# Performance work log

Hardware: AMD Instinct MI355X
Metric: run time of the kernel (lower is better)

## Reference

```python
import jax, jax.numpy as jnp
import numpy as np

B, S, V, E, H, MAX_OOVS = 32, 1024, 32000, 256, 512, 12
D2 = 2 * H + 100          # encoder feature dim after binary concat
IN = E + D2               # GRU input size


def setup_inputs() -> dict:
    key = jax.random.key(0)
    ks = jax.random.split(key, 18)
    sc = 0.02
    return {
        "input_idx": jax.random.randint(ks[0], (B,), 0, V),
        "encoded": jax.random.normal(ks[1], (B, S, 2 * H), jnp.float32),
        "encoded_idx": jax.random.randint(ks[2], (B, S), 0, V + MAX_OOVS),
        "prev_state": jax.random.normal(ks[3], (B, H), jnp.float32),
        "weighted": jax.random.normal(ks[4], (B, 1, D2), jnp.float32),
        "binary_vectors": jax.random.uniform(ks[5], (B, S, 1), jnp.float32),
        "order": 1,
        "embed_table": jax.random.normal(ks[6], (V, E), jnp.float32) * sc,
        "W_ih": jax.random.normal(ks[7], (3 * H, IN), jnp.float32) * sc,
        "b_ih": jax.random.normal(ks[8], (3 * H,), jnp.float32) * sc,
        "W_hh": jax.random.normal(ks[9], (3 * H, H), jnp.float32) * sc,
        "b_hh": jax.random.normal(ks[10], (3 * H,), jnp.float32) * sc,
        "Wo_w": jax.random.normal(ks[11], (V, H), jnp.float32) * sc,
        "Wo_b": jax.random.normal(ks[12], (V,), jnp.float32) * sc,
        "Wc_w": jax.random.normal(ks[13], (H, D2), jnp.float32) * sc,
        "Wc_b": jax.random.normal(ks[14], (H,), jnp.float32) * sc,
        "Ws_w": jax.random.normal(ks[15], (H, D2), jnp.float32) * sc,
        "Ws_b": jax.random.normal(ks[16], (H,), jnp.float32) * sc,
    }


def _gru_step(x, h, W_ih, b_ih, W_hh, b_hh):
    # torch nn.GRU single-step math
    gi = x @ W_ih.T + b_ih
    gh = h @ W_hh.T + b_hh
    i_r, i_z, i_n = jnp.split(gi, 3, axis=1)
    h_r, h_z, h_n = jnp.split(gh, 3, axis=1)
    r = jax.nn.sigmoid(i_r + h_r)
    z = jax.nn.sigmoid(i_z + h_z)
    n = jnp.tanh(i_n + r * h_n)
    return (1.0 - z) * n + z * h


def reference(input_idx, encoded, encoded_idx, prev_state, weighted,
              binary_vectors, order, embed_table, W_ih, b_ih, W_hh, b_hh,
              Wo_w, Wo_b, Wc_w, Wc_b, Ws_w, Ws_b):
    b, s = encoded.shape[0], encoded.shape[1]
    vocab = Wo_w.shape[0]
    # concat binary feature expanded to 100 channels -> (b, s, 2H+100)
    bin100 = jnp.broadcast_to(binary_vectors, (b, s, 100))
    enc = jnp.concatenate([encoded, bin100], axis=2)

    if order == 0:
        prev_state = enc[:, -1] @ Ws_w.T + Ws_b
        weighted = jnp.zeros((b, 1, enc.shape[2]), enc.dtype)

    emb = embed_table[input_idx][:, None, :]          # (b,1,E)
    x = jnp.concatenate([emb, weighted], axis=2)[:, 0]  # (b, IN)
    state = _gru_step(x, prev_state, W_ih, b_ih, W_hh, b_hh)  # (b,H)

    score_g = state @ Wo_w.T + Wo_b                   # (b, V)
    sc = jnp.tanh(enc @ Wc_w.T + Wc_b)                # (b, s, H)
    score_c = jnp.tanh(jnp.einsum('bsh,bh->bs', sc, state))
    score_c = score_c + jnp.where(encoded_idx == 0, -1000.0, 0.0).astype(score_c.dtype)

    probs = jax.nn.softmax(jnp.concatenate([score_g, score_c], axis=1), axis=1)
    prob_g = probs[:, :vocab]
    prob_c = probs[:, vocab:]
    prob_c_given = prob_c / jnp.sum(prob_c)           # faithful: scalar sum over all elems

    oovs = jnp.full((b, MAX_OOVS), 1e-4, probs.dtype)
    prob_g = jnp.concatenate([prob_g, oovs], axis=1)  # (b, V+OOV)

    # scatter-add copy probs into vocab space (same math as one_hot + bmm)
    rows = jnp.arange(b)[:, None]
    prob_c_to_g = jnp.zeros((b, vocab + MAX_OOVS), probs.dtype).at[rows, encoded_idx].add(prob_c)
    out = (prob_g + prob_c_to_g)[:, None, :]          # (b,1,V+OOV)

    idx_from = (encoded_idx == input_idx[:, None]).astype(probs.dtype)
    ssum = idx_from.sum(axis=1, keepdims=True)
    idx_from = jnp.where(ssum > 1, idx_from / ssum, idx_from)

    attn = prob_c_given * idx_from                    # (b, s)
    weighted_out = jnp.einsum('bs,bsd->bd', attn, enc)[:, None, :]
    return out, state, weighted_out
```

## Files before the change

### kernel.cpp

```cpp
#include <hip/hip_runtime.h>

#define B_   32
#define S_   1024
#define V_   32000
#define E_   256
#define H_   512
#define D2_  1124
#define IN_  1380
#define INP_ 1408
#define G3_  1536
#define VO_  32012
#define NKT_ 36

typedef __bf16 bf16x8 __attribute__((ext_vector_type(8)));
typedef float  f32x4  __attribute__((ext_vector_type(4)));

static __device__ __forceinline__ unsigned short f2bf(float f) {
    union { float f; unsigned int u; } v; v.f = f;
    unsigned int u = v.u;
    unsigned int r = (u + 0x7FFFu + ((u >> 16) & 1u)) >> 16;
    return (unsigned short)r;
}

static __device__ __forceinline__ unsigned int pkbf(unsigned int a, unsigned int b) {
    return ((a + 0x8000u) >> 16) | ((b + 0x8000u) & 0xffff0000u);
}

static __device__ __forceinline__ float tanh_fast(float x) {
    float e = __builtin_amdgcn_exp2f(x * 2.8853901817f);
    return 1.0f - 2.0f * __builtin_amdgcn_rcpf(e + 1.0f);
}

static __device__ __forceinline__ void glds16(const void* g, void* l) {
    __builtin_amdgcn_global_load_lds(
        (const __attribute__((address_space(1))) unsigned int*)g,
        (__attribute__((address_space(3))) unsigned int*)l, 16, 0, 0);
}

__global__ void k_prep(const int* order, const int* input_idx, const float* embed,
                       const float* weighted, const float* prev,
                       const float* encoded, const float* bin,
                       const float* Ws_w, const float* Ws_b,
                       float* x, float* prev_eff) {
    int b = blockIdx.x, t = threadIdx.x;
    int ord = order[0];
    const float* emb = embed + (size_t)input_idx[b] * E_;
    for (int d = t; d < INP_; d += 256) {
        float v;
        if (d < E_)       v = emb[d];
        else if (d < IN_) v = ord ? weighted[b * D2_ + (d - E_)] : 0.0f;
        else              v = 0.0f;
        x[b * INP_ + d] = v;
    }
    if (ord) {
        for (int i = t; i < H_; i += 256) prev_eff[b * H_ + i] = prev[b * H_ + i];
    } else {
        const float* encrow = encoded + ((size_t)(b * S_ + (S_ - 1))) * 1024;
        float bv = bin[b * S_ + (S_ - 1)];
        for (int h = t; h < H_; h += 256) {
            float acc = Ws_b[h];
            const float* wr = Ws_w + (size_t)h * D2_;
            for (int d = 0; d < 1024; d++) acc += encrow[d] * wr[d];
            for (int d = 1024; d < D2_; d++) acc += bv * wr[d];
            prev_eff[b * H_ + h] = acc;
        }
    }
}

__global__ void k_pack_wc(const float* Wc_w, unsigned short* bpack) {
    int idx = blockIdx.x * 256 + threadIdx.x;
    int j = idx & 7, lane = (idx >> 3) & 63, ht = (idx >> 9) & 31, kt = idx >> 14;
    int h = ht * 16 + (lane & 15);
    int k = kt * 32 + (lane >> 4) * 8 + j;
    float v = (k < D2_) ? Wc_w[(size_t)h * D2_ + k] : 0.0f;
    bpack[idx] = f2bf(v);
}

__global__ void k_gi(const float* x, const float* W_ih, const float* b_ih, float* gi) {
    extern __shared__ float smemF[];
    int t = threadIdx.x;
    int bh = blockIdx.x & 1;
    int hq = blockIdx.x >> 1;
    const float4* xg = (const float4*)(x + (size_t)bh * 16 * INP_);
    float4* xl4 = (float4*)smemF;
    for (int j = t; j < 16 * INP_ / 4; j += 256) xl4[j] = xg[j];
    __syncthreads();
    int w = t >> 6, l = t & 63;
    int h3 = hq * 4 + w;
    const float* wr = W_ih + (size_t)h3 * IN_;
    float4 wv[6];
#pragma unroll
    for (int i = 0; i < 6; i++) {
        int k = 4 * l + 256 * i;
        if (k + 3 < IN_) wv[i] = *(const float4*)(wr + k);
        else {
            float a0 = (k     < IN_) ? wr[k]     : 0.f;
            float a1 = (k + 1 < IN_) ? wr[k + 1] : 0.f;
            float a2 = (k + 2 < IN_) ? wr[k + 2] : 0.f;
            float a3 = (k + 3 < IN_) ? wr[k + 3] : 0.f;
            wv[i] = make_float4(a0, a1, a2, a3);
        }
    }
    float bias = b_ih[h3];
    for (int bb = 0; bb < 16; bb++) {
        const float4* xr = xl4 + bb * (INP_ / 4);
        float p = 0.f;
#pragma unroll
        for (int i = 0; i < 6; i++) {
            float4 xv = xr[l + 64 * i];
            p += wv[i].x * xv.x + wv[i].y * xv.y + wv[i].z * xv.z + wv[i].w * xv.w;
        }
#pragma unroll
        for (int off = 32; off >= 1; off >>= 1) p += __shfl_xor(p, off, 64);
        if (l == 0) gi[(bh * 16 + bb) * G3_ + h3] = p + bias;
    }
}

__global__ void k_gh(const float* prev_eff, const float* W_hh, const float* b_hh, float* gh) {
    extern __shared__ float smemF[];
    int t = threadIdx.x;
    const float4* pg = (const float4*)prev_eff;
    float4* pl4 = (float4*)smemF;
    for (int j = t; j < B_ * H_ / 4; j += 256) pl4[j] = pg[j];
    __syncthreads();
    int w = t >> 6, l = t & 63;
    int h3 = blockIdx.x * 4 + w;
    const float* wr = W_hh + (size_t)h3 * H_;
    float4 w0 = *(const float4*)(wr + 4 * l);
    float4 w1 = *(const float4*)(wr + 256 + 4 * l);
    float bias = b_hh[h3];
    for (int bb = 0; bb < B_; bb++) {
        const float* pr = smemF + bb * H_;
        float4 s0 = *(const float4*)(pr + 4 * l);
        float4 s1 = *(const float4*)(pr + 256 + 4 * l);
        float p = w0.x * s0.x + w0.y * s0.y + w0.z * s0.z + w0.w * s0.w
                + w1.x * s1.x + w1.y * s1.y + w1.z * s1.z + w1.w * s1.w;
#pragma unroll
        for (int off = 32; off >= 1; off >>= 1) p += __shfl_xor(p, off, 64);
        if (l == 0) gh[bb * G3_ + h3] = p + bias;
    }
}

__global__ void k_gate(const float* gi, const float* gh, const float* prev_eff,
                       float* state, float* out_state) {
    int idx = blockIdx.x * 256 + threadIdx.x;
    int b = idx >> 9, h = idx & 511;
    float ir = gi[b * G3_ + h],           hr = gh[b * G3_ + h];
    float iz = gi[b * G3_ + H_ + h],      hz = gh[b * G3_ + H_ + h];
    float in_ = gi[b * G3_ + 2 * H_ + h], hn = gh[b * G3_ + 2 * H_ + h];
    float r = 1.0f / (1.0f + expf(-(ir + hr)));
    float z = 1.0f / (1.0f + expf(-(iz + hz)));
    float n = tanhf(in_ + r * hn);
    float st = (1.0f - z) * n + z * prev_eff[idx];
    state[idx] = st;
    out_state[idx] = st;
}

__global__ void __launch_bounds__(256) k_scoreg(const float* state, const float* Wo_w,
                                                const float* Wo_b, float* scoreg) {
    __shared__ unsigned short Abf[32 * 520];
    int t = threadIdx.x;
    {
        int m = t & 31, g = t >> 5;
        const float4* src = (const float4*)(state + m * 512 + g * 64);
        unsigned short* dst = &Abf[m * 520 + g * 64];
#pragma unroll
        for (int i = 0; i < 16; i++) {
            float4 v = src[i];
            ushort4 p; p.x = f2bf(v.x); p.y = f2bf(v.y); p.z = f2bf(v.z); p.w = f2bf(v.w);
            *(ushort4*)(dst + i * 4) = p;
        }
    }
    __syncthreads();
    int w = t >> 6, l = t & 63;
    int q = l >> 4, m16 = l & 15;
    int n = blockIdx.x * 64 + w * 16 + m16;
    const uint4* wrow = (const uint4*)(Wo_w + (size_t)n * 512 + q * 8);
    f32x4 acc0 = {0.f, 0.f, 0.f, 0.f}, acc1 = {0.f, 0.f, 0.f, 0.f};
#pragma unroll
    for (int kt = 0; kt < 16; kt++) {
        uint4 w0 = wrow[kt * 8];
        uint4 w1 = wrow[kt * 8 + 1];
        int4 pb;
        pb.x = (int)pkbf(w0.x, w0.y); pb.y = (int)pkbf(w0.z, w0.w);
        pb.z = (int)pkbf(w1.x, w1.y); pb.w = (int)pkbf(w1.z, w1.w);
        bf16x8 bv = *(bf16x8*)&pb;
        bf16x8 a0 = *(const bf16x8*)&Abf[m16 * 520 + kt * 32 + q * 8];
        bf16x8 a1 = *(const bf16x8*)&Abf[(16 + m16) * 520 + kt * 32 + q * 8];
        acc0 = __builtin_amdgcn_mfma_f32_16x16x32_bf16(a0, bv, acc0, 0, 0, 0);
        acc1 = __builtin_amdgcn_mfma_f32_16x16x32_bf16(a1, bv, acc1, 0, 0, 0);
    }
    float wb = Wo_b[n];
#pragma unroll
    for (int r = 0; r < 4; r++) {
        scoreg[(q * 4 + r) * V_ + n]        = acc0[r] + wb;
        scoreg[(16 + q * 4 + r) * V_ + n]   = acc1[r] + wb;
    }
}

__global__ void __launch_bounds__(512) k_sc(
    const float* encoded, const float* bin, const unsigned short* bpack,
    const float* Wc_b, const float* state, const int* enc_idx, float* scorec) {
    __shared__ unsigned short Ab[2][2048];
    __shared__ unsigned short Bb[2][16384];
    __shared__ float partL[8][64];
    int t = threadIdx.x;
    int b  = blockIdx.x >> 4;
    int s0 = (blockIdx.x & 15) << 6;
    int w = t >> 6, l = t & 63;
    int q = l >> 4, m = l & 15;

    int ar = t >> 3, ak = (t & 7) * 4;
    const float* encrow = encoded + ((size_t)(b * S_ + s0 + ar)) * 1024 + ak;
    float binf = bin[b * S_ + s0 + ar];

    f32x4 acc[4][4];
#pragma unroll
    for (int i = 0; i < 4; i++)
#pragma unroll
        for (int j = 0; j < 4; j++) { acc[i][j][0]=0.f; acc[i][j][1]=0.f; acc[i][j][2]=0.f; acc[i][j][3]=0.f; }

    {
        float4 a0 = *(const float4*)encrow;
        ushort4 p; p.x = f2bf(a0.x); p.y = f2bf(a0.y); p.z = f2bf(a0.z); p.w = f2bf(a0.w);
        *(ushort4*)&Ab[0][ar * 32 + ak] = p;
#pragma unroll
        for (int i = 0; i < 4; i++)
            glds16(bpack + (size_t)((i * 8 + w) * 64 + l) * 8, &Bb[0][(i * 8 + w) * 512]);
    }
    float4 a1 = *(const float4*)(encrow + 32);
    __syncthreads();

#pragma unroll 2
    for (int kt = 0; kt < NKT_; kt++) {
        int cur = kt & 1;
        if (kt + 1 < NKT_) {
            int nx = cur ^ 1;
#pragma unroll
            for (int i = 0; i < 4; i++)
                glds16(bpack + (size_t)(kt + 1) * 16384 + (size_t)((i * 8 + w) * 64 + l) * 8,
                       &Bb[nx][(i * 8 + w) * 512]);
            ushort4 pn;
            if (kt + 1 < 32) {
                pn.x = f2bf(a1.x); pn.y = f2bf(a1.y); pn.z = f2bf(a1.z); pn.w = f2bf(a1.w);
            } else {
                int kb = (kt + 1) * 32 + ak;
                pn.x = f2bf(kb     < D2_ ? binf : 0.f);
                pn.y = f2bf(kb + 1 < D2_ ? binf : 0.f);
                pn.z = f2bf(kb + 2 < D2_ ? binf : 0.f);
                pn.w = f2bf(kb + 3 < D2_ ? binf : 0.f);
            }
            *(ushort4*)&Ab[nx][ar * 32 + ak] = pn;
            if (kt + 2 < 32) a1 = *(const float4*)(encrow + (kt + 2) * 32);
        }
        bf16x8 av[4], bv[4];
#pragma unroll
        for (int st = 0; st < 4; st++)
            av[st] = *(const bf16x8*)&Ab[cur][(st * 16 + m) * 32 + q * 8];
#pragma unroll
        for (int jj = 0; jj < 4; jj++)
            bv[jj] = *(const bf16x8*)&Bb[cur][((w * 4 + jj) * 64 + l) * 8];
#pragma unroll
        for (int st = 0; st < 4; st++)
#pragma unroll
            for (int jj = 0; jj < 4; jj++)
                acc[st][jj] = __builtin_amdgcn_mfma_f32_16x16x32_bf16(av[st], bv[jj], acc[st][jj], 0, 0, 0);
        __syncthreads();
    }

    float hb[4], hs[4];
#pragma unroll
    for (int jj = 0; jj < 4; jj++) {
        int h = (w * 4 + jj) * 16 + m;
        hb[jj] = Wc_b[h];
        hs[jj] = state[b * H_ + h];
    }
#pragma unroll
    for (int st = 0; st < 4; st++) {
#pragma unroll
        for (int r = 0; r < 4; r++) {
            float val = 0.f;
#pragma unroll
            for (int jj = 0; jj < 4; jj++)
                val += tanh_fast(acc[st][jj][r] + hb[jj]) * hs[jj];
            val += __shfl_xor(val, 1, 64);
            val += __shfl_xor(val, 2, 64);
            val += __shfl_xor(val, 4, 64);
            val += __shfl_xor(val, 8, 64);
            if (m == 0) partL[w][st * 16 + q * 4 + r] = val;
        }
    }
    __syncthreads();
    if (t < 64) {
        float tot = 0.f;
#pragma unroll
        for (int ww = 0; ww < 8; ww++) tot += partL[ww][t];
        int s = s0 + t;
        int ei = enc_idx[b * S_ + s];
        scorec[b * S_ + s] = tanh_fast(tot) + (ei == 0 ? -1000.0f : 0.0f);
    }
}

__global__ void k_exp(float* scoreg, float* scorec, float* partA, float* partC) {
    int blk = blockIdx.x;
    int b = blk / 17, c = blk % 17;
    int t = threadIdx.x;
    float sa = 0.f;
    if (c < 16) {
        int base = b * V_ + c * 2000;
        for (int i = t; i < 2000; i += 256) {
            float e = __expf(scoreg[base + i]);
            scoreg[base + i] = e;
            sa += e;
        }
    } else {
        int base = b * 1024;
        for (int i = t; i < 1024; i += 256) {
            float e = __expf(scorec[base + i]);
            scorec[base + i] = e;
            sa += e;
        }
    }
#pragma unroll
    for (int off = 32; off >= 1; off >>= 1) sa += __shfl_xor(sa, off, 64);
    __shared__ float rA[4];
    int w = t >> 6, l = t & 63;
    if (l == 0) rA[w] = sa;
    __syncthreads();
    if (t == 0) {
        float tot = rA[0] + rA[1] + rA[2] + rA[3];
        partA[blk] = tot;
        if (c == 16) partC[b] = tot;
    }
}

__global__ void k_combine(const float* partA, const float* partC, float* rowinv, float* invgc,
                          int* cnt, int* list, const int* enc_idx, const int* input_idx) {
    __shared__ float rs[32], rc[32];
    int t = threadIdx.x;
    if (t < 32) {
        float a = 0.f;
        for (int j = 0; j < 17; j++) a += partA[t * 17 + j];
        rs[t] = a; rc[t] = partC[t];
        rowinv[t] = 1.0f / a;
        cnt[t] = 0;
    }
    __syncthreads();
    if (t == 0) {
        float g = 0.f;
        for (int b = 0; b < 32; b++) g += rc[b] / rs[b];
        invgc[0] = 1.0f / g;
    }
    for (int i = t; i < B_ * S_; i += 512) {
        int b = i >> 10;
        if (enc_idx[i] == input_idx[b]) {
            int p = atomicAdd(&cnt[b], 1);
            list[b * S_ + p] = i & 1023;
        }
    }
}

__global__ void k_write(const float* scoreg, const float* scorec, const float* rowinv,
                        float* out, float* probc) {
    int idx = blockIdx.x * 256 + threadIdx.x;
    if (idx < B_ * V_) {
        int b = idx / V_, v = idx - b * V_;
        out[b * VO_ + v] = scoreg[idx] * rowinv[b];
    } else if (idx < B_ * V_ + B_ * S_) {
        int j = idx - B_ * V_;
        int b = j >> 10;
        probc[j] = scorec[j] * rowinv[b];
    } else {
        int j = idx - B_ * V_ - B_ * S_;
        if (j < B_ * 12) {
            int b = j / 12;
            out[b * VO_ + V_ + (j - b * 12)] = 0.0001f;
        }
    }
}

__global__ void k_scatter(const float* probc, const int* enc_idx, float* out) {
    int idx = blockIdx.x * 256 + threadIdx.x;
    int b = idx >> 10;
    atomicAdd(&out[b * VO_ + enc_idx[idx]], probc[idx]);
}

__global__ void k_wo(const float* probc, const int* list, const int* cnt, const float* invgc,
                     const float* encoded, const float* bin, float* out2) {
    int b = blockIdx.x, t = threadIdx.x;
    __shared__ float aL[1024];
    __shared__ int   sL[1024];
    int n = cnt[b];
    float scale = invgc[0] * (n > 1 ? 1.0f / (float)n : 1.0f);
    for (int i = t; i < n; i += 256) {
        int s = list[b * S_ + i];
        sL[i] = s;
        aL[i] = probc[b * S_ + s] * scale;
    }
    __syncthreads();
    for (int d = t; d < D2_; d += 256) {
        float acc = 0.f;
        for (int i = 0; i < n; i++) {
            int s = sL[i];
            float ev = (d < 1024) ? encoded[((size_t)(b * S_ + s)) * 1024 + d] : bin[b * S_ + s];
            acc += aL[i] * ev;
        }
        out2[b * D2_ + d] = acc;
    }
}

extern "C" void kernel_launch(void* const* d_in, const int* in_sizes, int n_in,
                              void* d_out, int out_size, void* d_ws, size_t ws_size,
                              hipStream_t stream) {
    const int*   input_idx = (const int*)d_in[0];
    const float* encoded   = (const float*)d_in[1];
    const int*   enc_idx   = (const int*)d_in[2];
    const float* prev      = (const float*)d_in[3];
    const float* weighted  = (const float*)d_in[4];
    const float* bin       = (const float*)d_in[5];
    const int*   order     = (const int*)d_in[6];
    const float* embed     = (const float*)d_in[7];
    const float* W_ih      = (const float*)d_in[8];
    const float* b_ih      = (const float*)d_in[9];
    const float* W_hh      = (const float*)d_in[10];
    const float* b_hh      = (const float*)d_in[11];
    const float* Wo_w      = (const float*)d_in[12];
    const float* Wo_b      = (const float*)d_in[13];
    const float* Wc_w      = (const float*)d_in[14];
    const float* Wc_b      = (const float*)d_in[15];
    const float* Ws_w      = (const float*)d_in[16];
    const float* Ws_b      = (const float*)d_in[17];

    float* out  = (float*)d_out;
    float* out1 = out + B_ * VO_;
    float* out2 = out1 + B_ * H_;

    float* ws_f     = (float*)d_ws;
    float* w_state  = ws_f;
    float* w_prev   = ws_f + 16384;
    float* w_x      = ws_f + 68736;
    float* w_gi     = ws_f + 113792;
    float* w_gh     = ws_f + 162944;
    float* w_scoreg = ws_f + 212096;
    float* w_scorec = ws_f + 1236096;
    float* w_probc  = ws_f + 1268864;
    float* w_partA  = ws_f + 1301632;
    float* w_partC  = ws_f + 1302176;
    float* w_rowinv = ws_f + 1302208;
    float* w_invgc  = ws_f + 1302240;
    int*   w_cnt    = (int*)(ws_f + 1302248);
    int*   w_list   = w_cnt + 32;
    unsigned short* w_bpack = (unsigned short*)(ws_f + 1335048);

    k_prep<<<32, 256, 0, stream>>>(order, input_idx, embed, weighted, prev,
                                   encoded, bin, Ws_w, Ws_b, w_x, w_prev);
    k_pack_wc<<<2304, 256, 0, stream>>>(Wc_w, w_bpack);
    k_gi<<<768, 256, 16 * INP_ * sizeof(float), stream>>>(w_x, W_ih, b_ih, w_gi);
    k_gh<<<384, 256, B_ * H_ * sizeof(float), stream>>>(w_prev, W_hh, b_hh, w_gh);
    k_gate<<<64, 256, 0, stream>>>(w_gi, w_gh, w_prev, w_state, out1);
    k_scoreg<<<500, 256, 0, stream>>>(w_state, Wo_w, Wo_b, w_scoreg);
    k_sc<<<512, 512, 0, stream>>>(encoded, bin, w_bpack, Wc_b, w_state, enc_idx, w_scorec);
    k_exp<<<544, 256, 0, stream>>>(w_scoreg, w_scorec, w_partA, w_partC);
    k_combine<<<1, 512, 0, stream>>>(w_partA, w_partC, w_rowinv, w_invgc, w_cnt, w_list, enc_idx, input_idx);
    k_write<<<4130, 256, 0, stream>>>(w_scoreg, w_scorec, w_rowinv, out, w_probc);
    k_scatter<<<128, 256, 0, stream>>>(w_probc, enc_idx, out);
    k_wo<<<32, 256, 0, stream>>>(w_probc, w_list, w_cnt, w_invgc, encoded, bin, out2);
}
```

Measured before the change: 440.4 us.

## Load Wc weight fragments directly from global and widen A tile to 128-K stages in k_sc

Drops LDS staging of the packed Wc weight tile in k_sc; each wave now reads its bf16 B fragments straight from global/L2. The encoded A tile is staged in LDS in 128-wide K chunks with a padded row stride of 136, which cuts barriers from 36 to 9 iterations. Launch bounds now request 4 blocks per CU, made possible by the much smaller LDS footprint. The trade-off is B loads that are no longer double-buffered and come from global memory on the critical path, plus heavier register pressure.

```diff
diff --git a/kernel.cpp b/kernel.cpp
--- a/kernel.cpp
+++ b/kernel.cpp
@@ -10,7 +10,6 @@
 #define INP_ 1408
 #define G3_  1536
 #define VO_  32012
-#define NKT_ 36
 
 typedef __bf16 bf16x8 __attribute__((ext_vector_type(8)));
 typedef float  f32x4  __attribute__((ext_vector_type(4)));
@@ -29,12 +28,6 @@
 static __device__ __forceinline__ float tanh_fast(float x) {
     float e = __builtin_amdgcn_exp2f(x * 2.8853901817f);
     return 1.0f - 2.0f * __builtin_amdgcn_rcpf(e + 1.0f);
-}
-
-static __device__ __forceinline__ void glds16(const void* g, void* l) {
-    __builtin_amdgcn_global_load_lds(
-        (const __attribute__((address_space(1))) unsigned int*)g,
-        (__attribute__((address_space(3))) unsigned int*)l, 16, 0, 0);
 }
 
 __global__ void k_prep(const int* order, const int* input_idx, const float* embed,
@@ -198,11 +191,10 @@
     }
 }
 
-__global__ void __launch_bounds__(512) k_sc(
+__global__ void __launch_bounds__(512, 4) k_sc(
     const float* encoded, const float* bin, const unsigned short* bpack,
     const float* Wc_b, const float* state, const int* enc_idx, float* scorec) {
-    __shared__ unsigned short Ab[2][2048];
-    __shared__ unsigned short Bb[2][16384];
+    __shared__ unsigned short Ab[2][64 * 136];
     __shared__ float partL[8][64];
     int t = threadIdx.x;
     int b  = blockIdx.x >> 4;
@@ -210,9 +202,11 @@
     int w = t >> 6, l = t & 63;
     int q = l >> 4, m = l & 15;
 
-    int ar = t >> 3, ak = (t & 7) * 4;
-    const float* encrow = encoded + ((size_t)(b * S_ + s0 + ar)) * 1024 + ak;
-    float binf = bin[b * S_ + s0 + ar];
+    int r = t >> 3, kg = t & 7;
+    const float* encbase = encoded + ((size_t)(b * S_ + s0 + r)) * 1024 + kg * 16;
+    float binf = bin[b * S_ + s0 + r];
+    unsigned short* dst0 = &Ab[0][r * 136 + kg * 16];
+    unsigned short* dst1 = &Ab[1][r * 136 + kg * 16];
 
     f32x4 acc[4][4];
 #pragma unroll
@@ -220,51 +214,54 @@
 #pragma unroll
         for (int j = 0; j < 4; j++) { acc[i][j][0]=0.f; acc[i][j][1]=0.f; acc[i][j][2]=0.f; acc[i][j][3]=0.f; }
 
-    {
-        float4 a0 = *(const float4*)encrow;
-        ushort4 p; p.x = f2bf(a0.x); p.y = f2bf(a0.y); p.z = f2bf(a0.z); p.w = f2bf(a0.w);
-        *(ushort4*)&Ab[0][ar * 32 + ak] = p;
-#pragma unroll
-        for (int i = 0; i < 4; i++)
-            glds16(bpack + (size_t)((i * 8 + w) * 64 + l) * 8, &Bb[0][(i * 8 + w) * 512]);
-    }
-    float4 a1 = *(const float4*)(encrow + 32);
-    __syncthreads();
-
-#pragma unroll 2
-    for (int kt = 0; kt < NKT_; kt++) {
-        int cur = kt & 1;
-        if (kt + 1 < NKT_) {
-            int nx = cur ^ 1;
-#pragma unroll
-            for (int i = 0; i < 4; i++)
-                glds16(bpack + (size_t)(kt + 1) * 16384 + (size_t)((i * 8 + w) * 64 + l) * 8,
-                       &Bb[nx][(i * 8 + w) * 512]);
-            ushort4 pn;
-            if (kt + 1 < 32) {
-                pn.x = f2bf(a1.x); pn.y = f2bf(a1.y); pn.z = f2bf(a1.z); pn.w = f2bf(a1.w);
-            } else {
-                int kb = (kt + 1) * 32 + ak;
-                pn.x = f2bf(kb     < D2_ ? binf : 0.f);
-                pn.y = f2bf(kb + 1 < D2_ ? binf : 0.f);
-                pn.z = f2bf(kb + 2 < D2_ ? binf : 0.f);
-                pn.w = f2bf(kb + 3 < D2_ ? binf : 0.f);
+    float4 ap[4];
+#pragma unroll
+    for (int j = 0; j < 4; j++) ap[j] = *(const float4*)(encbase + j * 4);
+
+    for (int s = 0; s < 9; s++) {
+        unsigned short* dst = (s & 1) ? dst1 : dst0;
+        if (s < 8) {
+#pragma unroll
+            for (int j = 0; j < 4; j++) {
+                ushort4 p;
+                p.x = f2bf(ap[j].x); p.y = f2bf(ap[j].y);
+                p.z = f2bf(ap[j].z); p.w = f2bf(ap[j].w);
+                *(ushort4*)(dst + j * 4) = p;
             }
-            *(ushort4*)&Ab[nx][ar * 32 + ak] = pn;
-            if (kt + 2 < 32) a1 = *(const float4*)(encrow + (kt + 2) * 32);
-        }
-        bf16x8 av[4], bv[4];
-#pragma unroll
-        for (int st = 0; st < 4; st++)
-            av[st] = *(const bf16x8*)&Ab[cur][(st * 16 + m) * 32 + q * 8];
-#pragma unroll
-        for (int jj = 0; jj < 4; jj++)
-            bv[jj] = *(const bf16x8*)&Bb[cur][((w * 4 + jj) * 64 + l) * 8];
-#pragma unroll
-        for (int st = 0; st < 4; st++)
+        } else {
+#pragma unroll
+            for (int j = 0; j < 4; j++) {
+                int kb = kg * 16 + j * 4;
+                ushort4 p;
+                p.x = f2bf(kb     < 100 ? binf : 0.f);
+                p.y = f2bf(kb + 1 < 100 ? binf : 0.f);
+                p.z = f2bf(kb + 2 < 100 ? binf : 0.f);
+                p.w = f2bf(kb + 3 < 100 ? binf : 0.f);
+                *(ushort4*)(dst + j * 4) = p;
+            }
+        }
+        __syncthreads();
+        if (s < 7) {
+#pragma unroll
+            for (int j = 0; j < 4; j++) ap[j] = *(const float4*)(encbase + (s + 1) * 128 + j * 4);
+        }
+        const unsigned short* abase = &Ab[s & 1][m * 136 + q * 8];
+#pragma unroll
+        for (int sub = 0; sub < 4; sub++) {
+            int kt = s * 4 + sub;
+            bf16x8 bv[4], av[4];
 #pragma unroll
             for (int jj = 0; jj < 4; jj++)
-                acc[st][jj] = __builtin_amdgcn_mfma_f32_16x16x32_bf16(av[st], bv[jj], acc[st][jj], 0, 0, 0);
+                bv[jj] = *(const bf16x8*)&bpack[(((size_t)kt * 32 + (w * 4 + jj)) * 64 + l) * 8];
+#pragma unroll
+            for (int st = 0; st < 4; st++)
+                av[st] = *(const bf16x8*)(abase + st * 16 * 136 + sub * 32);
+#pragma unroll
+            for (int st = 0; st < 4; st++)
+#pragma unroll
+                for (int jj = 0; jj < 4; jj++)
+                    acc[st][jj] = __builtin_amdgcn_mfma_f32_16x16x32_bf16(av[st], bv[jj], acc[st][jj], 0, 0, 0);
+        }
         __syncthreads();
     }
 
@@ -278,16 +275,16 @@
 #pragma unroll
     for (int st = 0; st < 4; st++) {
 #pragma unroll
-        for (int r = 0; r < 4; r++) {
+        for (int rr = 0; rr < 4; rr++) {
             float val = 0.f;
 #pragma unroll
             for (int jj = 0; jj < 4; jj++)
-                val += tanh_fast(acc[st][jj][r] + hb[jj]) * hs[jj];
+                val += tanh_fast(acc[st][jj][rr] + hb[jj]) * hs[jj];
             val += __shfl_xor(val, 1, 64);
             val += __shfl_xor(val, 2, 64);
             val += __shfl_xor(val, 4, 64);
             val += __shfl_xor(val, 8, 64);
-            if (m == 0) partL[w][st * 16 + q * 4 + r] = val;
+            if (m == 0) partL[w][st * 16 + q * 4 + rr] = val;
         }
     }
     __syncthreads();
```

Result: no change. 439.9 us (-0.1%).
